# Optimization experiments

Hardware: AMD Instinct MI355X
Metric: run time of the kernel (lower is better)

The kernel has to match this reference:

```python
import jax, jax.numpy as jnp
import numpy as np

B, S, D, H = 2, 2048, 1024, 16
HD = D // H
NEG = -10000.0


def setup_inputs() -> dict:
    key = jax.random.key(0)
    ks = jax.random.split(key, 9)
    # xavier-uniform-like scale for square d_model x d_model weights
    lim = float(np.sqrt(6.0 / (D + D)))
    mk_w = lambda k: jax.random.uniform(k, (D, D), jnp.float32, -lim, lim)
    return {
        "q": jax.random.normal(ks[0], (B, S, D), jnp.float32),
        "k": jax.random.normal(ks[1], (B, S, D), jnp.float32),
        "v": jax.random.normal(ks[2], (B, S, D), jnp.float32),
        "attn_mask": jax.random.randint(ks[3], (B, S), 0, 2, jnp.int32),
        "Wq": mk_w(ks[4]),
        "Wk": mk_w(ks[5]),
        "Wv": mk_w(ks[6]),
        "Wo": mk_w(ks[7]),
        "mask_future": 1,
    }


def reference(q, k, v, attn_mask, Wq, Wk, Wv, Wo, mask_future):
    # nn.Linear(bias=False): y = x @ W.T
    def split_heads(x, W):
        return (x @ W.T).reshape(B, S, H, HD).transpose(0, 2, 1, 3)  # [B,H,S,HD]

    qh = split_heads(q, Wq)
    kh = split_heads(k, Wk)
    vh = split_heads(v, Wv)

    scale = 1.0 / np.sqrt(HD)
    scores = jnp.einsum("bhld,bhsd->bhls", qh, kh) * scale  # [B,H,L,S]

    if mask_future:  # static python flag
        rows = jnp.arange(S)[:, None]
        cols = jnp.arange(S)[None, :]
        causal_bias = jnp.where(cols > rows, jnp.float32(NEG), jnp.float32(0.0))
        scores = scores + causal_bias

    # masked_fill(attn_mask == 0, -10000): sets score exactly to NEG (after bias add)
    pad = attn_mask[:, None, None, :]  # [B,1,1,S]
    scores = jnp.where(pad == 0, jnp.float32(NEG), scores)

    probs = jax.nn.softmax(scores, axis=-1)
    ctx = jnp.einsum("bhls,bhsd->bhld", probs, vh)  # [B,H,L,HD]
    ctx = ctx.transpose(0, 2, 1, 3).reshape(B, S, D)
    return ctx @ Wo.T
```

## Files before the change

kernel.cpp:

```cpp
#include <hip/hip_runtime.h>
#include <hip/hip_bf16.h>

typedef __attribute__((ext_vector_type(8))) short bf16x8;
typedef __attribute__((ext_vector_type(4))) short bf16x4;
typedef __attribute__((ext_vector_type(4))) float f32x4;

#define B_ 2
#define S_ 2048
#define D_ 1024
#define H_ 16
#define HD_ 64
#define M_ 4096
#define NEGV (-10000.0f)

#define NQ_ 4194304
#define NW_ 1048576

#if __has_builtin(__builtin_amdgcn_mfma_f32_16x16x16bf16_1k)
#define HAVE_MFMA16 1
#else
#define HAVE_MFMA16 0
#endif

static __device__ __forceinline__ unsigned short f2bf(float x) {
  __hip_bfloat16 h = __float2bfloat16(x);
  return *reinterpret_cast<unsigned short*>(&h);
}

static __device__ __forceinline__ float bf2f(unsigned short u) {
  unsigned int x = ((unsigned int)u) << 16;
  return __uint_as_float(x);
}

static __device__ __forceinline__ bf16x8 cvt8(const float* p) {
  float4 a = *reinterpret_cast<const float4*>(p);
  float4 b = *reinterpret_cast<const float4*>(p + 4);
  bf16x8 r;
  r[0] = (short)f2bf(a.x); r[1] = (short)f2bf(a.y);
  r[2] = (short)f2bf(a.z); r[3] = (short)f2bf(a.w);
  r[4] = (short)f2bf(b.x); r[5] = (short)f2bf(b.y);
  r[6] = (short)f2bf(b.z); r[7] = (short)f2bf(b.w);
  return r;
}

static __device__ __forceinline__ void gl_lds16(const unsigned short* g, unsigned short* l) {
#if __has_builtin(__builtin_amdgcn_global_load_lds)
  __builtin_amdgcn_global_load_lds(
      (const __attribute__((address_space(1))) unsigned int*)g,
      (__attribute__((address_space(3))) unsigned int*)l, 16, 0, 0);
#else
  *reinterpret_cast<bf16x8*>(l) = *reinterpret_cast<const bf16x8*>(g);
#endif
}


__global__ __launch_bounds__(256) void cvt_all(const float* __restrict__ q,
                                               const float* __restrict__ k,
                                               const float* __restrict__ v,
                                               const float* __restrict__ wq,
                                               const float* __restrict__ wk,
                                               const float* __restrict__ wv,
                                               const float* __restrict__ wo,
                                               unsigned short* __restrict__ dst) {
  for (size_t c = (size_t)blockIdx.x * 256 + threadIdx.x; c < 2097152; c += (size_t)2048 * 256) {
    const size_t e = c * 8;
    const float* s;
    if (e < (size_t)NQ_)            s = q  + e;
    else if (e < (size_t)2 * NQ_)   s = k  + (e - (size_t)NQ_);
    else if (e < (size_t)3 * NQ_)   s = v  + (e - (size_t)2 * NQ_);
    else if (e < (size_t)3 * NQ_ + NW_)     s = wq + (e - (size_t)3 * NQ_);
    else if (e < (size_t)3 * NQ_ + 2 * NW_) s = wk + (e - (size_t)3 * NQ_ - NW_);
    else if (e < (size_t)3 * NQ_ + 3 * NW_) s = wv + (e - (size_t)3 * NQ_ - 2 * NW_);
    else                                    s = wo + (e - (size_t)3 * NQ_ - 3 * NW_);
    *reinterpret_cast<bf16x8*>(dst + e) = cvt8(s);
  }
}

template<bool HSPLIT>
static __device__ __forceinline__ void core_fast(const unsigned short* A,
                                                 const unsigned short* Bw,
                                                 unsigned short* Asm, unsigned short* Bsm,
                                                 int m0, int n0, f32x4 (*acc)[4]) {
  const int tid = threadIdx.x, lane = tid & 63, wid = tid >> 6;
  const int wm = wid >> 1, wn = wid & 1;
  const int l15 = lane & 15, l4 = lane >> 4;

  for (int k0 = 0; k0 < 1024; k0 += 64) {
    __syncthreads();
#pragma unroll
    for (int i = 0; i < 4; ++i) {
      const int idx = tid + 256 * i;
      const int row = idx >> 3;
      const int ce = ((idx & 7) * 8) ^ ((row & 7) << 3);
      const unsigned short* ga;
      if constexpr (HSPLIT) {
        const int m = m0 + row, kk = k0 + ce;
        const int bb = m >> 11, s = m & 2047;
        ga = A + (((size_t)(bb * H_ + (kk >> 6)) * S_ + s) * HD_ + (kk & 63));
      } else {
        ga = A + (size_t)(m0 + row) * 1024 + k0 + ce;
      }
      gl_lds16(ga, Asm + (size_t)idx * 8);
      gl_lds16(Bw + (size_t)(n0 + row) * 1024 + k0 + ce, Bsm + (size_t)idx * 8);
    }
    __syncthreads();
#pragma unroll
    for (int kk = 0; kk < 2; ++kk) {
      bf16x8 af[4], bfr[4];
#pragma unroll
      for (int f = 0; f < 4; ++f) {
        const int ra = wm * 64 + f * 16 + l15;
        const int ca = (kk * 32 + l4 * 8) ^ ((ra & 7) << 3);
        af[f] = *reinterpret_cast<const bf16x8*>(&Asm[ra * 64 + ca]);
        const int rb = wn * 64 + f * 16 + l15;
        const int cb = (kk * 32 + l4 * 8) ^ ((rb & 7) << 3);
        bfr[f] = *reinterpret_cast<const bf16x8*>(&Bsm[rb * 64 + cb]);
      }
#pragma unroll
      for (int fm = 0; fm < 4; ++fm)
#pragma unroll
        for (int fn = 0; fn < 4; ++fn)
          acc[fm][fn] = __builtin_amdgcn_mfma_f32_16x16x32_bf16(af[fm], bfr[fn], acc[fm][fn], 0, 0, 0);
    }
  }
}

__global__ __launch_bounds__(256) void gemm_qkv_fast(const unsigned short* __restrict__ qbf,
                                                     const unsigned short* __restrict__ kbf,
                                                     const unsigned short* __restrict__ vbf,
                                                     const unsigned short* __restrict__ wbf,
                                                     unsigned short* __restrict__ Qh,
                                                     unsigned short* __restrict__ Kh,
                                                     unsigned short* __restrict__ Vt) {
  __shared__ unsigned short Asm[128 * 64];
  __shared__ unsigned short Bsm[128 * 64];
  const int z = blockIdx.z;
  const unsigned short* A  = (z == 0) ? qbf : (z == 1) ? kbf : vbf;
  const unsigned short* Bw = wbf + (size_t)z * NW_;
  const int m0 = blockIdx.y * 128, n0 = blockIdx.x * 128;
  const int lane = threadIdx.x & 63, wid = threadIdx.x >> 6;
  const int wm = wid >> 1, wn = wid & 1;
  const int l15 = lane & 15, l4 = lane >> 4;
  f32x4 acc[4][4] = {};
  core_fast<false>(A, Bw, Asm, Bsm, m0, n0, acc);

#pragma unroll
  for (int fm = 0; fm < 4; ++fm) {
#pragma unroll
    for (int fn = 0; fn < 4; ++fn) {
      const int mg0 = m0 + wm * 64 + fm * 16 + l4 * 4;
      const int ng  = n0 + wn * 64 + fn * 16 + l15;
      const int bidx = mg0 >> 11, s = mg0 & 2047;
      const int h = ng >> 6, d = ng & 63;
      if (z < 2) {
        unsigned short* C = (z == 0) ? Qh : Kh;
#pragma unroll
        for (int r = 0; r < 4; ++r)
          C[((size_t)((bidx * H_ + h) * S_ + s + r)) * HD_ + d] = f2bf(acc[fm][fn][r]);
      } else {
        ushort4 pk;
        pk.x = f2bf(acc[fm][fn][0]); pk.y = f2bf(acc[fm][fn][1]);
        pk.z = f2bf(acc[fm][fn][2]); pk.w = f2bf(acc[fm][fn][3]);
        *reinterpret_cast<ushort4*>(&Vt[((size_t)((bidx * H_ + h) * HD_ + d)) * S_ + s]) = pk;
      }
    }
  }
}

__global__ __launch_bounds__(256) void gemm_o_fast(const unsigned short* __restrict__ ctx,
                                                   const unsigned short* __restrict__ wobf,
                                                   float* __restrict__ Cout) {
  __shared__ unsigned short Asm[128 * 64];
  __shared__ unsigned short Bsm[128 * 64];
  const int m0 = blockIdx.y * 128, n0 = blockIdx.x * 128;
  const int lane = threadIdx.x & 63, wid = threadIdx.x >> 6;
  const int wm = wid >> 1, wn = wid & 1;
  const int l15 = lane & 15, l4 = lane >> 4;
  f32x4 acc[4][4] = {};
  core_fast<true>(ctx, wobf, Asm, Bsm, m0, n0, acc);

#pragma unroll
  for (int fm = 0; fm < 4; ++fm)
#pragma unroll
    for (int fn = 0; fn < 4; ++fn) {
      const int mg0 = m0 + wm * 64 + fm * 16 + l4 * 4;
      const int ng  = n0 + wn * 64 + fn * 16 + l15;
#pragma unroll
      for (int r = 0; r < 4; ++r)
        Cout[(size_t)(mg0 + r) * 1024 + ng] = acc[fm][fn][r];
    }
}

__global__ __launch_bounds__(128) void attn_split(const unsigned short* __restrict__ Qh,
                                                  const unsigned short* __restrict__ Kh,
                                                  const unsigned short* __restrict__ Vt,
                                                  const int* __restrict__ attn_mask,
                                                  const int* __restrict__ mask_future,
                                                  float* __restrict__ Pml,
                                                  unsigned short* __restrict__ Po) {
  constexpr int KVB = 64;
  __shared__ unsigned short Ksm[64 * 64];
  __shared__ unsigned short Vsm[64 * 64];
  __shared__ int s_any;
  const int bx = (int)blockIdx.x;
  int qt, part, bh;
  if (bx < 512)       { part = 0; qt = 16 + (bx >> 5); bh = bx & 31; }
  else if (bx < 544)  { part = 0; qt = 15;             bh = bx & 31; }
  else if (bx < 576)  { part = 1; qt = 31;             bh = bx & 31; }
  else if (bx < 1536) { const int j = bx - 576, g = j >> 6, n = 15 - g, r = j & 63;
                        if (r < 32) { part = 0; qt = n - 1;  bh = r; }
                        else        { part = 1; qt = n + 15; bh = r - 32; } }
  else                { const int j = bx - 1536; part = 1; qt = j >> 5; bh = j & 31; }

  const int q0 = qt * 64;
  const int tid = threadIdx.x, lane = tid & 63, wid = tid >> 6;
  const int l15 = lane & 15, l4 = lane >> 4;
  const int b = bh >> 4;
  const bool causal = (mask_future[0] != 0);
  const int* mrow = attn_mask + b * S_;

  if (tid == 0) s_any = 0;
  __syncthreads();
  for (int i = tid; i <= q0; i += 128)
    if (mrow[i]) s_any = 1;
  __syncthreads();
  const int kb_end_full = (causal && s_any) ? (q0 + 64) : S_;
  const int kb_lo = part ? 1024 : 0;
  const int kb_hi = part ? kb_end_full : (kb_end_full < 1024 ? kb_end_full : 1024);

  const unsigned short* Qb = Qh + (size_t)bh * S_ * HD_;
  const unsigned short* Kb = Kh + (size_t)bh * S_ * HD_;
  const unsigned short* Vb = Vt + (size_t)bh * HD_ * S_;

  float m_run[2] = {-1e30f, -1e30f}, l_run[2] = {0.f, 0.f};
  f32x4 o[2][4] = {};

  if (kb_lo < kb_hi) {
    int qrow[2];
    bf16x8 qf0[2], qf1[2];
#pragma unroll
    for (int f = 0; f < 2; ++f) {
      qrow[f] = q0 + wid * 32 + f * 16 + l15;
      qf0[f] = *reinterpret_cast<const bf16x8*>(&Qb[(size_t)qrow[f] * HD_ + l4 * 8]);
      qf1[f] = *reinterpret_cast<const bf16x8*>(&Qb[(size_t)qrow[f] * HD_ + 32 + l4 * 8]);
    }

    bf16x8 kreg[4], vreg[4];
#pragma unroll
    for (int j = 0; j < 4; ++j) {
      const int idx = tid + 128 * j;
      const int row = idx >> 3;
      const int ce = ((idx & 7) * 8) ^ ((row & 7) << 3);
      kreg[j] = *reinterpret_cast<const bf16x8*>(&Kb[(size_t)(kb_lo + row) * HD_ + ce]);
      vreg[j] = *reinterpret_cast<const bf16x8*>(&Vb[(size_t)row * S_ + kb_lo + ce]);
    }

    for (int kb = kb_lo; kb < kb_hi; kb += KVB) {
      __syncthreads();
#pragma unroll
      for (int j = 0; j < 4; ++j) {
        const int idx = tid + 128 * j;
        *reinterpret_cast<bf16x8*>(&Ksm[idx * 8]) = kreg[j];
        *reinterpret_cast<bf16x8*>(&Vsm[idx * 8]) = vreg[j];
      }
      __syncthreads();

      if (kb + KVB < kb_hi) {
        const int kn = kb + KVB;
#pragma unroll
        for (int j = 0; j < 4; ++j) {
          const int idx = tid + 128 * j;
          const int row = idx >> 3;
          const int ce = ((idx & 7) * 8) ^ ((row & 7) << 3);
          kreg[j] = *reinterpret_cast<const bf16x8*>(&Kb[(size_t)(kn + row) * HD_ + ce]);
          vreg[j] = *reinterpret_cast<const bf16x8*>(&Vb[(size_t)row * S_ + kn + ce]);
        }
      }

      int4 mk4[4];
#pragma unroll
      for (int nf = 0; nf < 4; ++nf)
        mk4[nf] = *reinterpret_cast<const int4*>(&mrow[kb + nf * 16 + l4 * 4]);

#pragma unroll
      for (int f = 0; f < 2; ++f) {
        f32x4 sc[4];
#pragma unroll
        for (int nf = 0; nf < 4; ++nf) {
          const int ra = nf * 16 + l15, sw = (ra & 7) << 3;
          bf16x8 kf0 = *reinterpret_cast<const bf16x8*>(&Ksm[ra * 64 + ((l4 * 8) ^ sw)]);
          bf16x8 kf1 = *reinterpret_cast<const bf16x8*>(&Ksm[ra * 64 + ((32 + l4 * 8) ^ sw)]);
          f32x4 z = {};
          z = __builtin_amdgcn_mfma_f32_16x16x32_bf16(kf0, qf0[f], z, 0, 0, 0);
          z = __builtin_amdgcn_mfma_f32_16x16x32_bf16(kf1, qf1[f], z, 0, 0, 0);
          sc[nf] = z;
        }

        float p[4][4];
        float mx = -1e30f;
#pragma unroll
        for (int nf = 0; nf < 4; ++nf) {
          const int kbase = kb + nf * 16 + l4 * 4;
#pragma unroll
          for (int r = 0; r < 4; ++r) {
            float vv = sc[nf][r] * 0.125f;
            if (causal && (kbase + r) > qrow[f]) vv += NEGV;
            const int mkr = (r == 0) ? mk4[nf].x : (r == 1) ? mk4[nf].y : (r == 2) ? mk4[nf].z : mk4[nf].w;
            if (mkr == 0) vv = NEGV;
            p[nf][r] = vv;
            mx = fmaxf(mx, vv);
          }
        }
        mx = fmaxf(mx, __shfl_xor(mx, 16));
        mx = fmaxf(mx, __shfl_xor(mx, 32));
        const float m_new = fmaxf(m_run[f], mx);
        const float scale = __expf(m_run[f] - m_new);
        float s_loc = 0.f;
#pragma unroll
        for (int nf = 0; nf < 4; ++nf)
#pragma unroll
          for (int r = 0; r < 4; ++r) {
            float e = __expf(p[nf][r] - m_new);
            p[nf][r] = e;
            s_loc += e;
          }
        s_loc += __shfl_xor(s_loc, 16);
        s_loc += __shfl_xor(s_loc, 32);
        l_run[f] = l_run[f] * scale + s_loc;
        m_run[f] = m_new;

        float sq[4];
#pragma unroll
        for (int r = 0; r < 4; ++r) sq[r] = __shfl(scale, l4 * 4 + r);
#pragma unroll
        for (int nf2 = 0; nf2 < 4; ++nf2)
#pragma unroll
          for (int r = 0; r < 4; ++r) o[f][nf2][r] *= sq[r];

        bf16x4 pk[4];
#pragma unroll
        for (int nf = 0; nf < 4; ++nf) {
          bf16x4 t;
          t[0] = (short)f2bf(p[nf][0]); t[1] = (short)f2bf(p[nf][1]);
          t[2] = (short)f2bf(p[nf][2]); t[3] = (short)f2bf(p[nf][3]);
          pk[nf] = t;
        }
#pragma unroll
        for (int nf2 = 0; nf2 < 4; ++nf2) {
          const int rv = nf2 * 16 + l15, swv = (rv & 7) << 3;
#pragma unroll
          for (int nf = 0; nf < 4; ++nf) {
            bf16x4 vf = *reinterpret_cast<const bf16x4*>(&Vsm[rv * 64 + ((nf * 16 + l4 * 4) ^ swv)]);
            o[f][nf2] = __builtin_amdgcn_mfma_f32_16x16x16bf16_1k(pk[nf], vf, o[f][nf2], 0, 0, 0);
          }
        }
      }
    }
  }

#pragma unroll
  for (int f = 0; f < 2; ++f) {
    const int row0 = q0 + wid * 32 + f * 16;
    if (l4 == 0) {
      float* pml = &Pml[(((size_t)bh * S_ + row0 + l15) * 2 + part) * 2];
      pml[0] = m_run[f];
      pml[1] = l_run[f];
    }
#pragma unroll
    for (int nf2 = 0; nf2 < 4; ++nf2)
#pragma unroll
      for (int r = 0; r < 4; ++r) {
        const int row = row0 + l4 * 4 + r;
        Po[(((size_t)bh * S_ + row) * 2 + part) * 64 + nf2 * 16 + l15] = f2bf(o[f][nf2][r]);
      }
  }
}

__global__ __launch_bounds__(256) void attn_combine(const float* __restrict__ Pml,
                                                    const unsigned short* __restrict__ Po,
                                                    unsigned short* __restrict__ ctx) {
  const int t = (int)blockIdx.x * 256 + (int)threadIdx.x;
  const int d = t & 63;
  const size_t rb = (size_t)(t >> 6);
  const float mA = Pml[(rb * 2 + 0) * 2], lA = Pml[(rb * 2 + 0) * 2 + 1];
  const float mB = Pml[(rb * 2 + 1) * 2], lB = Pml[(rb * 2 + 1) * 2 + 1];
  const float ms = fmaxf(mA, mB);
  const float wA = __expf(mA - ms), wB = __expf(mB - ms);
  const float L = lA * wA + lB * wB;
  const float oA = bf2f(Po[(rb * 2 + 0) * 64 + d]);
  const float oB = bf2f(Po[(rb * 2 + 1) * 64 + d]);
  ctx[rb * 64 + d] = f2bf((oA * wA + oB * wB) / L);
}


template<bool AF32, bool BF32, bool HSPLIT>
static __device__ __forceinline__ void gemm_core(const void* Av, const void* Bv,
                                                 unsigned short* Asm, unsigned short* Bsm,
                                                 int m0, int n0, f32x4 (*acc)[4]) {
  constexpr int BK = 64, LDT = 72;
  constexpr int K = 1024;
  const int tid = threadIdx.x;
  const int lane = tid & 63, wid = tid >> 6;
  const int wm = wid >> 1, wn = wid & 1;
  const int l15 = lane & 15, l4 = lane >> 4;

  for (int k0 = 0; k0 < K; k0 += BK) {
    __syncthreads();
#pragma unroll
    for (int i = 0; i < 4; ++i) {
      int idx = tid + 256 * i;
      int row = idx >> 3, k8 = (idx & 7) * 8;
      bf16x8 va, vb;
      if constexpr (AF32) {
        va = cvt8((const float*)Av + (size_t)(m0 + row) * K + k0 + k8);
      } else if constexpr (HSPLIT) {
        const int m = m0 + row, kk = k0 + k8;
        const int bb = m >> 11, s = m & 2047;
        va = *reinterpret_cast<const bf16x8*>(
            (const unsigned short*)Av +
            (((size_t)(bb * H_ + (kk >> 6)) * S_ + s) * HD_ + (kk & 63)));
      } else {
        va = *reinterpret_cast<const bf16x8*>((const unsigned short*)Av + (size_t)(m0 + row) * K + k0 + k8);
      }
      if constexpr (BF32) {
        vb = cvt8((const float*)Bv + (size_t)(n0 + row) * K + k0 + k8);
      } else {
        vb = *reinterpret_cast<const bf16x8*>((const unsigned short*)Bv + (size_t)(n0 + row) * K + k0 + k8);
      }
      *reinterpret_cast<bf16x8*>(&Asm[row * LDT + k8]) = va;
      *reinterpret_cast<bf16x8*>(&Bsm[row * LDT + k8]) = vb;
    }
    __syncthreads();
#pragma unroll
    for (int kk = 0; kk < 2; ++kk) {
      bf16x8 af[4], bfr[4];
#pragma unroll
      for (int f = 0; f < 4; ++f) {
        af[f]  = *reinterpret_cast<const bf16x8*>(&Asm[(wm * 64 + f * 16 + l15) * LDT + kk * 32 + l4 * 8]);
        bfr[f] = *reinterpret_cast<const bf16x8*>(&Bsm[(wn * 64 + f * 16 + l15) * LDT + kk * 32 + l4 * 8]);
      }
#pragma unroll
      for (int fm = 0; fm < 4; ++fm)
#pragma unroll
        for (int fn = 0; fn < 4; ++fn)
          acc[fm][fn] = __builtin_amdgcn_mfma_f32_16x16x32_bf16(af[fm], bfr[fn], acc[fm][fn], 0, 0, 0);
    }
  }
}

__global__ __launch_bounds__(256) void gemm_qkv3(const float* __restrict__ q,
                                                 const float* __restrict__ k,
                                                 const float* __restrict__ v,
                                                 const float* __restrict__ Wq,
                                                 const float* __restrict__ Wk,
                                                 const float* __restrict__ Wv,
                                                 unsigned short* __restrict__ Qh,
                                                 unsigned short* __restrict__ Kh,
                                                 unsigned short* __restrict__ Vt) {
  constexpr int LDT = 72;
  __shared__ unsigned short Asm[128 * LDT];
  __shared__ unsigned short Bsm[128 * LDT];
  const int z = blockIdx.z;
  const float* A  = (z == 0) ? q  : (z == 1) ? k  : v;
  const float* Bw = (z == 0) ? Wq : (z == 1) ? Wk : Wv;
  const int m0 = blockIdx.y * 128, n0 = blockIdx.x * 128;
  const int lane = threadIdx.x & 63, wid = threadIdx.x >> 6;
  const int wm = wid >> 1, wn = wid & 1;
  const int l15 = lane & 15, l4 = lane >> 4;
  f32x4 acc[4][4] = {};
  gemm_core<true, true, false>(A, Bw, Asm, Bsm, m0, n0, acc);

#pragma unroll
  for (int fm = 0; fm < 4; ++fm) {
#pragma unroll
    for (int fn = 0; fn < 4; ++fn) {
      const int mg0 = m0 + wm * 64 + fm * 16 + l4 * 4;
      const int ng  = n0 + wn * 64 + fn * 16 + l15;
      const int bidx = mg0 >> 11, s = mg0 & 2047;
      const int h = ng >> 6, d = ng & 63;
      if (z < 2) {
        unsigned short* C = (z == 0) ? Qh : Kh;
#pragma unroll
        for (int r = 0; r < 4; ++r)
          C[((size_t)((bidx * H_ + h) * S_ + s + r)) * HD_ + d] = f2bf(acc[fm][fn][r]);
      } else {
        ushort4 pk;
        pk.x = f2bf(acc[fm][fn][0]); pk.y = f2bf(acc[fm][fn][1]);
        pk.z = f2bf(acc[fm][fn][2]); pk.w = f2bf(acc[fm][fn][3]);
        *reinterpret_cast<ushort4*>(&Vt[((size_t)((bidx * H_ + h) * HD_ + d)) * S_ + s]) = pk;
      }
    }
  }
}

__global__ __launch_bounds__(256) void gemm_oproj(const void* __restrict__ Av,
                                                  const void* __restrict__ Bv,
                                                  float* __restrict__ Cout) {
  constexpr int LDT = 72;
  __shared__ unsigned short Asm[128 * LDT];
  __shared__ unsigned short Bsm[128 * LDT];
  const int m0 = blockIdx.y * 128, n0 = blockIdx.x * 128;
  const int lane = threadIdx.x & 63, wid = threadIdx.x >> 6;
  const int wm = wid >> 1, wn = wid & 1;
  const int l15 = lane & 15, l4 = lane >> 4;
  f32x4 acc[4][4] = {};
  gemm_core<false, true, true>(Av, Bv, Asm, Bsm, m0, n0, acc);

#pragma unroll
  for (int fm = 0; fm < 4; ++fm)
#pragma unroll
    for (int fn = 0; fn < 4; ++fn) {
      const int mg0 = m0 + wm * 64 + fm * 16 + l4 * 4;
      const int ng  = n0 + wn * 64 + fn * 16 + l15;
#pragma unroll
      for (int r = 0; r < 4; ++r)
        Cout[(size_t)(mg0 + r) * 1024 + ng] = acc[fm][fn][r];
    }
}

__global__ __launch_bounds__(128) void attn_fwd(const unsigned short* Qh,
                                                const unsigned short* __restrict__ Kh,
                                                const unsigned short* __restrict__ Vt,
                                                const int* __restrict__ attn_mask,
                                                const int* __restrict__ mask_future,
                                                unsigned short* ctx) {
  constexpr int KVB = 64;
  __shared__ unsigned short Ksm[64 * 64];
  __shared__ unsigned short Vsm[64 * 64];
  __shared__ int s_any;
  const int tid = threadIdx.x, lane = tid & 63, wid = tid >> 6;
  const int l15 = lane & 15, l4 = lane >> 4;
  const int bh = blockIdx.y, b = bh >> 4;
  const int q0 = (int)((blockIdx.x + 9 * blockIdx.y) & 31) * 64;
  const bool causal = (mask_future[0] != 0);
  const int* mrow = attn_mask + b * S_;

  if (tid == 0) s_any = 0;
  __syncthreads();
  for (int i = tid; i <= q0; i += 128)
    if (mrow[i]) s_any = 1;
  __syncthreads();
  const int kb_end = (causal && s_any) ? (q0 + 64) : S_;

  const unsigned short* Qb = Qh + (size_t)bh * S_ * HD_;
  const unsigned short* Kb = Kh + (size_t)bh * S_ * HD_;
  const unsigned short* Vb = Vt + (size_t)bh * HD_ * S_;

  int qrow[2];
  bf16x8 qf0[2], qf1[2];
#pragma unroll
  for (int f = 0; f < 2; ++f) {
    qrow[f] = q0 + wid * 32 + f * 16 + l15;
    qf0[f] = *reinterpret_cast<const bf16x8*>(&Qb[(size_t)qrow[f] * HD_ + l4 * 8]);
    qf1[f] = *reinterpret_cast<const bf16x8*>(&Qb[(size_t)qrow[f] * HD_ + 32 + l4 * 8]);
  }

  float m_run[2] = {-1e30f, -1e30f}, l_run[2] = {0.f, 0.f};
  f32x4 o[2][4] = {};

  bf16x8 kreg[4], vreg[4];
#pragma unroll
  for (int j = 0; j < 4; ++j) {
    const int idx = tid + 128 * j;
    const int row = idx >> 3;
    const int ce = ((idx & 7) * 8) ^ ((row & 7) << 3);
    kreg[j] = *reinterpret_cast<const bf16x8*>(&Kb[(size_t)row * HD_ + ce]);
    vreg[j] = *reinterpret_cast<const bf16x8*>(&Vb[(size_t)row * S_ + ce]);
  }

  for (int kb = 0; kb < kb_end; kb += KVB) {
    __syncthreads();
#pragma unroll
    for (int j = 0; j < 4; ++j) {
      const int idx = tid + 128 * j;
      *reinterpret_cast<bf16x8*>(&Ksm[idx * 8]) = kreg[j];
      *reinterpret_cast<bf16x8*>(&Vsm[idx * 8]) = vreg[j];
    }
    __syncthreads();

    if (kb + KVB < kb_end) {
      const int kn = kb + KVB;
#pragma unroll
      for (int j = 0; j < 4; ++j) {
        const int idx = tid + 128 * j;
        const int row = idx >> 3;
        const int ce = ((idx & 7) * 8) ^ ((row & 7) << 3);
        kreg[j] = *reinterpret_cast<const bf16x8*>(&Kb[(size_t)(kn + row) * HD_ + ce]);
        vreg[j] = *reinterpret_cast<const bf16x8*>(&Vb[(size_t)row * S_ + kn + ce]);
      }
    }

    int4 mk4[4];
#pragma unroll
    for (int nf = 0; nf < 4; ++nf)
      mk4[nf] = *reinterpret_cast<const int4*>(&mrow[kb + nf * 16 + l4 * 4]);

#pragma unroll
    for (int f = 0; f < 2; ++f) {
      f32x4 sc[4];
#pragma unroll
      for (int nf = 0; nf < 4; ++nf) {
        const int ra = nf * 16 + l15, sw = (ra & 7) << 3;
        bf16x8 kf0 = *reinterpret_cast<const bf16x8*>(&Ksm[ra * 64 + ((l4 * 8) ^ sw)]);
        bf16x8 kf1 = *reinterpret_cast<const bf16x8*>(&Ksm[ra * 64 + ((32 + l4 * 8) ^ sw)]);
        f32x4 z = {};
        z = __builtin_amdgcn_mfma_f32_16x16x32_bf16(kf0, qf0[f], z, 0, 0, 0);
        z = __builtin_amdgcn_mfma_f32_16x16x32_bf16(kf1, qf1[f], z, 0, 0, 0);
        sc[nf] = z;
      }

      float p[4][4];
      float mx = -1e30f;
#pragma unroll
      for (int nf = 0; nf < 4; ++nf) {
        const int kbase = kb + nf * 16 + l4 * 4;
#pragma unroll
        for (int r = 0; r < 4; ++r) {
          float vv = sc[nf][r] * 0.125f;
          if (causal && (kbase + r) > qrow[f]) vv += NEGV;
          const int mkr = (r == 0) ? mk4[nf].x : (r == 1) ? mk4[nf].y : (r == 2) ? mk4[nf].z : mk4[nf].w;
          if (mkr == 0) vv = NEGV;
          p[nf][r] = vv;
          mx = fmaxf(mx, vv);
        }
      }
      mx = fmaxf(mx, __shfl_xor(mx, 16));
      mx = fmaxf(mx, __shfl_xor(mx, 32));
      const float m_new = fmaxf(m_run[f], mx);
      const float scale = __expf(m_run[f] - m_new);
      float s_loc = 0.f;
#pragma unroll
      for (int nf = 0; nf < 4; ++nf)
#pragma unroll
        for (int r = 0; r < 4; ++r) {
          float e = __expf(p[nf][r] - m_new);
          p[nf][r] = e;
          s_loc += e;
        }
      s_loc += __shfl_xor(s_loc, 16);
      s_loc += __shfl_xor(s_loc, 32);
      l_run[f] = l_run[f] * scale + s_loc;
      m_run[f] = m_new;

      float sq[4];
#pragma unroll
      for (int r = 0; r < 4; ++r) sq[r] = __shfl(scale, l4 * 4 + r);
#pragma unroll
      for (int nf2 = 0; nf2 < 4; ++nf2)
#pragma unroll
        for (int r = 0; r < 4; ++r) o[f][nf2][r] *= sq[r];

      bf16x4 pk[4];
#pragma unroll
      for (int nf = 0; nf < 4; ++nf) {
        bf16x4 t;
        t[0] = (short)f2bf(p[nf][0]); t[1] = (short)f2bf(p[nf][1]);
        t[2] = (short)f2bf(p[nf][2]); t[3] = (short)f2bf(p[nf][3]);
        pk[nf] = t;
      }
#pragma unroll
      for (int nf2 = 0; nf2 < 4; ++nf2) {
        const int rv = nf2 * 16 + l15, swv = (rv & 7) << 3;
#pragma unroll
        for (int nf = 0; nf < 4; ++nf) {
          bf16x4 vf = *reinterpret_cast<const bf16x4*>(&Vsm[rv * 64 + ((nf * 16 + l4 * 4) ^ swv)]);
          o[f][nf2] = __builtin_amdgcn_mfma_f32_16x16x16bf16_1k(pk[nf], vf, o[f][nf2], 0, 0, 0);
        }
      }
    }
  }

#pragma unroll
  for (int f = 0; f < 2; ++f) {
    const float linv = 1.f / l_run[f];
    float lq[4];
#pragma unroll
    for (int r = 0; r < 4; ++r) lq[r] = __shfl(linv, l4 * 4 + r);
#pragma unroll
    for (int nf2 = 0; nf2 < 4; ++nf2)
#pragma unroll
      for (int r = 0; r < 4; ++r) {
        const int rowg = q0 + wid * 32 + f * 16 + l4 * 4 + r;
        ctx[((size_t)bh * S_ + rowg) * HD_ + nf2 * 16 + l15] = f2bf(o[f][nf2][r] * lq[r]);
      }
  }
}

extern "C" void kernel_launch(void* const* d_in, const int* in_sizes, int n_in,
                              void* d_out, int out_size, void* d_ws, size_t ws_size,
                              hipStream_t stream) {
  const float* q = (const float*)d_in[0];
  const float* k = (const float*)d_in[1];
  const float* v = (const float*)d_in[2];
  const int* attn_mask = (const int*)d_in[3];
  const float* Wq = (const float*)d_in[4];
  const float* Wk = (const float*)d_in[5];
  const float* Wv = (const float*)d_in[6];
  const float* Wo = (const float*)d_in[7];
  const int* mask_future = (const int*)d_in[8];

  unsigned short* ws = (unsigned short*)d_ws;
  unsigned short* Vt = (unsigned short*)d_out;
  float* out = (float*)d_out;
  (void)in_sizes; (void)n_in; (void)out_size;

  const size_t CVT_ELEMS = (size_t)3 * NQ_ + 4 * NW_;
  const size_t NEED = (CVT_ELEMS + 2 * (size_t)NQ_) * 2;

  if (ws_size >= NEED) {
    unsigned short* cvt = ws;
    unsigned short* qbf = cvt;
    unsigned short* kbf = cvt + (size_t)NQ_;
    unsigned short* vbf = cvt + (size_t)2 * NQ_;
    unsigned short* wbf = cvt + (size_t)3 * NQ_;
    unsigned short* Qh  = cvt + CVT_ELEMS;
    unsigned short* Kh  = Qh + (size_t)NQ_;
    float* Pml = (float*)d_ws;
    unsigned short* Po = (unsigned short*)((char*)d_ws + (1 << 20));

    cvt_all<<<2048, 256, 0, stream>>>(q, k, v, Wq, Wk, Wv, Wo, cvt);
    gemm_qkv_fast<<<dim3(8, 32, 3), 256, 0, stream>>>(qbf, kbf, vbf, wbf, Qh, Kh, Vt);
    attn_split<<<2048, 128, 0, stream>>>(Qh, Kh, Vt, attn_mask, mask_future, Pml, Po);
    attn_combine<<<16384, 256, 0, stream>>>(Pml, Po, Qh);
    gemm_o_fast<<<dim3(8, 32), 256, 0, stream>>>(Qh, wbf + (size_t)3 * NW_, out);
  } else {
    unsigned short* Qh = ws;
    unsigned short* Kh = ws + (size_t)NQ_;
    gemm_qkv3<<<dim3(8, 32, 3), 256, 0, stream>>>(q, k, v, Wq, Wk, Wv, Qh, Kh, Vt);
    attn_fwd<<<dim3(32, 32), 128, 0, stream>>>(Qh, Kh, Vt, attn_mask, mask_future, Qh);
    gemm_oproj<<<dim3(8, 32), 256, 0, stream>>>(Qh, Wo, out);
  }
}
```

Measured before the change: 175.8 us.

## Use atomic work queue and three-way KV split in attention

The attention kernel now pulls jobs from a global atomic counter instead of mapping a fixed job to each block. A separate tiny kernel zeroes the counter before launch. The KV range is split into three 768-key chunks rather than two halves, and jobs are ordered longest-first to balance the causal workload across CUs. The combine kernel merges three partial softmax states instead of two, and the partial buffers are relocated into the dead bf16 input region. The cost is more partial-result traffic, atomic contention and an extra launch.

```diff
diff --git a/kernel.cpp b/kernel.cpp
--- a/kernel.cpp
+++ b/kernel.cpp
@@ -15,12 +15,7 @@
 
 #define NQ_ 4194304
 #define NW_ 1048576
-
-#if __has_builtin(__builtin_amdgcn_mfma_f32_16x16x16bf16_1k)
-#define HAVE_MFMA16 1
-#else
-#define HAVE_MFMA16 0
-#endif
+#define NJOBS 3072
 
 static __device__ __forceinline__ unsigned short f2bf(float x) {
   __hip_bfloat16 h = __float2bfloat16(x);
@@ -191,188 +186,200 @@
     }
 }
 
+__global__ void zero_ctr(unsigned int* c) { *c = 0; }
+
 __global__ __launch_bounds__(128) void attn_split(const unsigned short* __restrict__ Qh,
                                                   const unsigned short* __restrict__ Kh,
                                                   const unsigned short* __restrict__ Vt,
                                                   const int* __restrict__ attn_mask,
                                                   const int* __restrict__ mask_future,
                                                   float* __restrict__ Pml,
-                                                  unsigned short* __restrict__ Po) {
+                                                  unsigned short* __restrict__ Po,
+                                                  unsigned int* __restrict__ ctr) {
   constexpr int KVB = 64;
   __shared__ unsigned short Ksm[64 * 64];
   __shared__ unsigned short Vsm[64 * 64];
-  __shared__ int s_any;
-  const int bx = (int)blockIdx.x;
-  int qt, part, bh;
-  if (bx < 512)       { part = 0; qt = 16 + (bx >> 5); bh = bx & 31; }
-  else if (bx < 544)  { part = 0; qt = 15;             bh = bx & 31; }
-  else if (bx < 576)  { part = 1; qt = 31;             bh = bx & 31; }
-  else if (bx < 1536) { const int j = bx - 576, g = j >> 6, n = 15 - g, r = j & 63;
-                        if (r < 32) { part = 0; qt = n - 1;  bh = r; }
-                        else        { part = 1; qt = n + 15; bh = r - 32; } }
-  else                { const int j = bx - 1536; part = 1; qt = j >> 5; bh = j & 31; }
-
-  const int q0 = qt * 64;
+  __shared__ int s_job, s_any;
   const int tid = threadIdx.x, lane = tid & 63, wid = tid >> 6;
   const int l15 = lane & 15, l4 = lane >> 4;
-  const int b = bh >> 4;
   const bool causal = (mask_future[0] != 0);
-  const int* mrow = attn_mask + b * S_;
-
-  if (tid == 0) s_any = 0;
-  __syncthreads();
-  for (int i = tid; i <= q0; i += 128)
-    if (mrow[i]) s_any = 1;
-  __syncthreads();
-  const int kb_end_full = (causal && s_any) ? (q0 + 64) : S_;
-  const int kb_lo = part ? 1024 : 0;
-  const int kb_hi = part ? kb_end_full : (kb_end_full < 1024 ? kb_end_full : 1024);
-
-  const unsigned short* Qb = Qh + (size_t)bh * S_ * HD_;
-  const unsigned short* Kb = Kh + (size_t)bh * S_ * HD_;
-  const unsigned short* Vb = Vt + (size_t)bh * HD_ * S_;
-
-  float m_run[2] = {-1e30f, -1e30f}, l_run[2] = {0.f, 0.f};
-  f32x4 o[2][4] = {};
-
-  if (kb_lo < kb_hi) {
-    int qrow[2];
-    bf16x8 qf0[2], qf1[2];
-#pragma unroll
-    for (int f = 0; f < 2; ++f) {
-      qrow[f] = q0 + wid * 32 + f * 16 + l15;
-      qf0[f] = *reinterpret_cast<const bf16x8*>(&Qb[(size_t)qrow[f] * HD_ + l4 * 8]);
-      qf1[f] = *reinterpret_cast<const bf16x8*>(&Qb[(size_t)qrow[f] * HD_ + 32 + l4 * 8]);
-    }
-
-    bf16x8 kreg[4], vreg[4];
-#pragma unroll
-    for (int j = 0; j < 4; ++j) {
-      const int idx = tid + 128 * j;
-      const int row = idx >> 3;
-      const int ce = ((idx & 7) * 8) ^ ((row & 7) << 3);
-      kreg[j] = *reinterpret_cast<const bf16x8*>(&Kb[(size_t)(kb_lo + row) * HD_ + ce]);
-      vreg[j] = *reinterpret_cast<const bf16x8*>(&Vb[(size_t)row * S_ + kb_lo + ce]);
-    }
-
-    for (int kb = kb_lo; kb < kb_hi; kb += KVB) {
-      __syncthreads();
-#pragma unroll
-      for (int j = 0; j < 4; ++j) {
-        const int idx = tid + 128 * j;
-        *reinterpret_cast<bf16x8*>(&Ksm[idx * 8]) = kreg[j];
-        *reinterpret_cast<bf16x8*>(&Vsm[idx * 8]) = vreg[j];
-      }
-      __syncthreads();
-
-      if (kb + KVB < kb_hi) {
-        const int kn = kb + KVB;
-#pragma unroll
-        for (int j = 0; j < 4; ++j) {
-          const int idx = tid + 128 * j;
-          const int row = idx >> 3;
-          const int ce = ((idx & 7) * 8) ^ ((row & 7) << 3);
-          kreg[j] = *reinterpret_cast<const bf16x8*>(&Kb[(size_t)(kn + row) * HD_ + ce]);
-          vreg[j] = *reinterpret_cast<const bf16x8*>(&Vb[(size_t)row * S_ + kn + ce]);
+
+  for (;;) {
+    __syncthreads();
+    if (tid == 0) s_job = (int)atomicAdd(ctr, 1u);
+    __syncthreads();
+    const int g = s_job;
+    if (g >= NJOBS) break;
+    const int bh = g & 31, j = g >> 5, b = bh >> 4;
+
+    int qt, p;
+    if (j < 21)      { p = 0; qt = 11 + j; }
+    else if (j < 30) { p = 1; qt = 2 + j; }
+    else if (j < 36) { const int L = 11 - ((j - 30) >> 1); p = (j - 30) & 1;
+                       qt = p ? 11 + L : L - 1; }
+    else if (j < 60) { const int jj = j - 36, L = 8 - jj / 3, pp = jj % 3;
+                       p = pp; qt = (pp == 0) ? L - 1 : (pp == 1) ? 11 + L : 23 + L; }
+    else if (j < 72) { p = 1; qt = j - 60; }
+    else             { p = 2; qt = j - 72; }
+
+    const int q0 = qt * 64;
+    const int* mrow = attn_mask + b * S_;
+
+    if (tid == 0) s_any = 0;
+    __syncthreads();
+    for (int i = tid; i <= q0; i += 128)
+      if (mrow[i]) s_any = 1;
+    __syncthreads();
+    const int kb_end_full = (causal && s_any) ? (q0 + 64) : S_;
+    const int kb_lo = p * 768;
+    const int kb_hi = (kb_lo + 768 < kb_end_full) ? (kb_lo + 768) : kb_end_full;
+
+    const unsigned short* Qb = Qh + (size_t)bh * S_ * HD_;
+    const unsigned short* Kb = Kh + (size_t)bh * S_ * HD_;
+    const unsigned short* Vb = Vt + (size_t)bh * HD_ * S_;
+
+    float m_run[2] = {-1e30f, -1e30f}, l_run[2] = {0.f, 0.f};
+    f32x4 o[2][4] = {};
+
+    if (kb_lo < kb_hi) {
+      int qrow[2];
+      bf16x8 qf0[2], qf1[2];
+#pragma unroll
+      for (int f = 0; f < 2; ++f) {
+        qrow[f] = q0 + wid * 32 + f * 16 + l15;
+        qf0[f] = *reinterpret_cast<const bf16x8*>(&Qb[(size_t)qrow[f] * HD_ + l4 * 8]);
+        qf1[f] = *reinterpret_cast<const bf16x8*>(&Qb[(size_t)qrow[f] * HD_ + 32 + l4 * 8]);
+      }
+
+      bf16x8 kreg[4], vreg[4];
+#pragma unroll
+      for (int jj = 0; jj < 4; ++jj) {
+        const int idx = tid + 128 * jj;
+        const int row = idx >> 3;
+        const int ce = ((idx & 7) * 8) ^ ((row & 7) << 3);
+        kreg[jj] = *reinterpret_cast<const bf16x8*>(&Kb[(size_t)(kb_lo + row) * HD_ + ce]);
+        vreg[jj] = *reinterpret_cast<const bf16x8*>(&Vb[(size_t)row * S_ + kb_lo + ce]);
+      }
+
+      for (int kb = kb_lo; kb < kb_hi; kb += KVB) {
+        __syncthreads();
+#pragma unroll
+        for (int jj = 0; jj < 4; ++jj) {
+          const int idx = tid + 128 * jj;
+          *reinterpret_cast<bf16x8*>(&Ksm[idx * 8]) = kreg[jj];
+          *reinterpret_cast<bf16x8*>(&Vsm[idx * 8]) = vreg[jj];
         }
-      }
-
-      int4 mk4[4];
-#pragma unroll
-      for (int nf = 0; nf < 4; ++nf)
-        mk4[nf] = *reinterpret_cast<const int4*>(&mrow[kb + nf * 16 + l4 * 4]);
-
-#pragma unroll
-      for (int f = 0; f < 2; ++f) {
-        f32x4 sc[4];
-#pragma unroll
-        for (int nf = 0; nf < 4; ++nf) {
-          const int ra = nf * 16 + l15, sw = (ra & 7) << 3;
-          bf16x8 kf0 = *reinterpret_cast<const bf16x8*>(&Ksm[ra * 64 + ((l4 * 8) ^ sw)]);
-          bf16x8 kf1 = *reinterpret_cast<const bf16x8*>(&Ksm[ra * 64 + ((32 + l4 * 8) ^ sw)]);
-          f32x4 z = {};
-          z = __builtin_amdgcn_mfma_f32_16x16x32_bf16(kf0, qf0[f], z, 0, 0, 0);
-          z = __builtin_amdgcn_mfma_f32_16x16x32_bf16(kf1, qf1[f], z, 0, 0, 0);
-          sc[nf] = z;
-        }
-
-        float p[4][4];
-        float mx = -1e30f;
-#pragma unroll
-        for (int nf = 0; nf < 4; ++nf) {
-          const int kbase = kb + nf * 16 + l4 * 4;
-#pragma unroll
-          for (int r = 0; r < 4; ++r) {
-            float vv = sc[nf][r] * 0.125f;
-            if (causal && (kbase + r) > qrow[f]) vv += NEGV;
-            const int mkr = (r == 0) ? mk4[nf].x : (r == 1) ? mk4[nf].y : (r == 2) ? mk4[nf].z : mk4[nf].w;
-            if (mkr == 0) vv = NEGV;
-            p[nf][r] = vv;
-            mx = fmaxf(mx, vv);
+        __syncthreads();
+
+        if (kb + KVB < kb_hi) {
+          const int kn = kb + KVB;
+#pragma unroll
+          for (int jj = 0; jj < 4; ++jj) {
+            const int idx = tid + 128 * jj;
+            const int row = idx >> 3;
+            const int ce = ((idx & 7) * 8) ^ ((row & 7) << 3);
+            kreg[jj] = *reinterpret_cast<const bf16x8*>(&Kb[(size_t)(kn + row) * HD_ + ce]);
+            vreg[jj] = *reinterpret_cast<const bf16x8*>(&Vb[(size_t)row * S_ + kn + ce]);
           }
         }
-        mx = fmaxf(mx, __shfl_xor(mx, 16));
-        mx = fmaxf(mx, __shfl_xor(mx, 32));
-        const float m_new = fmaxf(m_run[f], mx);
-        const float scale = __expf(m_run[f] - m_new);
-        float s_loc = 0.f;
+
+        int4 mk4[4];
 #pragma unroll
         for (int nf = 0; nf < 4; ++nf)
-#pragma unroll
-          for (int r = 0; r < 4; ++r) {
-            float e = __expf(p[nf][r] - m_new);
-            p[nf][r] = e;
-            s_loc += e;
+          mk4[nf] = *reinterpret_cast<const int4*>(&mrow[kb + nf * 16 + l4 * 4]);
+
+#pragma unroll
+        for (int f = 0; f < 2; ++f) {
+          f32x4 sc[4];
+#pragma unroll
+          for (int nf = 0; nf < 4; ++nf) {
+            const int ra = nf * 16 + l15, sw = (ra & 7) << 3;
+            bf16x8 kf0 = *reinterpret_cast<const bf16x8*>(&Ksm[ra * 64 + ((l4 * 8) ^ sw)]);
+            bf16x8 kf1 = *reinterpret_cast<const bf16x8*>(&Ksm[ra * 64 + ((32 + l4 * 8) ^ sw)]);
+            f32x4 z = {};
+            z = __builtin_amdgcn_mfma_f32_16x16x32_bf16(kf0, qf0[f], z, 0, 0, 0);
+            z = __builtin_amdgcn_mfma_f32_16x16x32_bf16(kf1, qf1[f], z, 0, 0, 0);
+            sc[nf] = z;
           }
-        s_loc += __shfl_xor(s_loc, 16);
-        s_loc += __shfl_xor(s_loc, 32);
-        l_run[f] = l_run[f] * scale + s_loc;
-        m_run[f] = m_new;
-
-        float sq[4];
-#pragma unroll
-        for (int r = 0; r < 4; ++r) sq[r] = __shfl(scale, l4 * 4 + r);
-#pragma unroll
-        for (int nf2 = 0; nf2 < 4; ++nf2)
-#pragma unroll
-          for (int r = 0; r < 4; ++r) o[f][nf2][r] *= sq[r];
-
-        bf16x4 pk[4];
-#pragma unroll
-        for (int nf = 0; nf < 4; ++nf) {
-          bf16x4 t;
-          t[0] = (short)f2bf(p[nf][0]); t[1] = (short)f2bf(p[nf][1]);
-          t[2] = (short)f2bf(p[nf][2]); t[3] = (short)f2bf(p[nf][3]);
-          pk[nf] = t;
-        }
-#pragma unroll
-        for (int nf2 = 0; nf2 < 4; ++nf2) {
-          const int rv = nf2 * 16 + l15, swv = (rv & 7) << 3;
+
+          float pp_[4][4];
+          float mx = -1e30f;
 #pragma unroll
           for (int nf = 0; nf < 4; ++nf) {
-            bf16x4 vf = *reinterpret_cast<const bf16x4*>(&Vsm[rv * 64 + ((nf * 16 + l4 * 4) ^ swv)]);
-            o[f][nf2] = __builtin_amdgcn_mfma_f32_16x16x16bf16_1k(pk[nf], vf, o[f][nf2], 0, 0, 0);
+            const int kbase = kb + nf * 16 + l4 * 4;
+#pragma unroll
+            for (int r = 0; r < 4; ++r) {
+              float vv = sc[nf][r] * 0.125f;
+              if (causal && (kbase + r) > qrow[f]) vv += NEGV;
+              const int mkr = (r == 0) ? mk4[nf].x : (r == 1) ? mk4[nf].y : (r == 2) ? mk4[nf].z : mk4[nf].w;
+              if (mkr == 0) vv = NEGV;
+              pp_[nf][r] = vv;
+              mx = fmaxf(mx, vv);
+            }
+          }
+          mx = fmaxf(mx, __shfl_xor(mx, 16));
+          mx = fmaxf(mx, __shfl_xor(mx, 32));
+          const float m_new = fmaxf(m_run[f], mx);
+          const float scale = __expf(m_run[f] - m_new);
+          float s_loc = 0.f;
+#pragma unroll
+          for (int nf = 0; nf < 4; ++nf)
+#pragma unroll
+            for (int r = 0; r < 4; ++r) {
+              float e = __expf(pp_[nf][r] - m_new);
+              pp_[nf][r] = e;
+              s_loc += e;
+            }
+          s_loc += __shfl_xor(s_loc, 16);
+          s_loc += __shfl_xor(s_loc, 32);
+          l_run[f] = l_run[f] * scale + s_loc;
+          m_run[f] = m_new;
+
+          float sq[4];
+#pragma unroll
+          for (int r = 0; r < 4; ++r) sq[r] = __shfl(scale, l4 * 4 + r);
+#pragma unroll
+          for (int nf2 = 0; nf2 < 4; ++nf2)
+#pragma unroll
+            for (int r = 0; r < 4; ++r) o[f][nf2][r] *= sq[r];
+
+          bf16x4 pk[4];
+#pragma unroll
+          for (int nf = 0; nf < 4; ++nf) {
+            bf16x4 t;
+            t[0] = (short)f2bf(pp_[nf][0]); t[1] = (short)f2bf(pp_[nf][1]);
+            t[2] = (short)f2bf(pp_[nf][2]); t[3] = (short)f2bf(pp_[nf][3]);
+            pk[nf] = t;
+          }
+#pragma unroll
+          for (int nf2 = 0; nf2 < 4; ++nf2) {
+            const int rv = nf2 * 16 + l15, swv = (rv & 7) << 3;
+#pragma unroll
+            for (int nf = 0; nf < 4; ++nf) {
+              bf16x4 vf = *reinterpret_cast<const bf16x4*>(&Vsm[rv * 64 + ((nf * 16 + l4 * 4) ^ swv)]);
+              o[f][nf2] = __builtin_amdgcn_mfma_f32_16x16x16bf16_1k(pk[nf], vf, o[f][nf2], 0, 0, 0);
+            }
           }
         }
       }
     }
-  }
-
-#pragma unroll
-  for (int f = 0; f < 2; ++f) {
-    const int row0 = q0 + wid * 32 + f * 16;
-    if (l4 == 0) {
-      float* pml = &Pml[(((size_t)bh * S_ + row0 + l15) * 2 + part) * 2];
-      pml[0] = m_run[f];
-      pml[1] = l_run[f];
-    }
-#pragma unroll
-    for (int nf2 = 0; nf2 < 4; ++nf2)
-#pragma unroll
-      for (int r = 0; r < 4; ++r) {
-        const int row = row0 + l4 * 4 + r;
-        Po[(((size_t)bh * S_ + row) * 2 + part) * 64 + nf2 * 16 + l15] = f2bf(o[f][nf2][r]);
-      }
+
+#pragma unroll
+    for (int f = 0; f < 2; ++f) {
+      const int row0 = q0 + wid * 32 + f * 16;
+      if (l4 == 0) {
+        float* pml = &Pml[(((size_t)bh * S_ + row0 + l15) * 3 + p) * 2];
+        pml[0] = m_run[f];
+        pml[1] = l_run[f];
+      }
+#pragma unroll
+      for (int nf2 = 0; nf2 < 4; ++nf2)
+#pragma unroll
+        for (int r = 0; r < 4; ++r) {
+          const int row = row0 + l4 * 4 + r;
+          Po[(((size_t)bh * S_ + row) * 3 + p) * 64 + nf2 * 16 + l15] = f2bf(o[f][nf2][r]);
+        }
+    }
   }
 }
 
@@ -382,14 +389,16 @@
   const int t = (int)blockIdx.x * 256 + (int)threadIdx.x;
   const int d = t & 63;
   const size_t rb = (size_t)(t >> 6);
-  const float mA = Pml[(rb * 2 + 0) * 2], lA = Pml[(rb * 2 + 0) * 2 + 1];
-  const float mB = Pml[(rb * 2 + 1) * 2], lB = Pml[(rb * 2 + 1) * 2 + 1];
-  const float ms = fmaxf(mA, mB);
-  const float wA = __expf(mA - ms), wB = __expf(mB - ms);
-  const float L = lA * wA + lB * wB;
-  const float oA = bf2f(Po[(rb * 2 + 0) * 64 + d]);
-  const float oB = bf2f(Po[(rb * 2 + 1) * 64 + d]);
-  ctx[rb * 64 + d] = f2bf((oA * wA + oB * wB) / L);
+  const float m0v = Pml[(rb * 3 + 0) * 2], l0 = Pml[(rb * 3 + 0) * 2 + 1];
+  const float m1v = Pml[(rb * 3 + 1) * 2], l1 = Pml[(rb * 3 + 1) * 2 + 1];
+  const float m2v = Pml[(rb * 3 + 2) * 2], l2 = Pml[(rb * 3 + 2) * 2 + 1];
+  const float ms = fmaxf(fmaxf(m0v, m1v), m2v);
+  const float w0 = __expf(m0v - ms), w1 = __expf(m1v - ms), w2 = __expf(m2v - ms);
+  const float L = l0 * w0 + l1 * w1 + l2 * w2;
+  const float o0 = bf2f(Po[(rb * 3 + 0) * 64 + d]);
+  const float o1 = bf2f(Po[(rb * 3 + 1) * 64 + d]);
+  const float o2 = bf2f(Po[(rb * 3 + 2) * 64 + d]);
+  ctx[rb * 64 + d] = f2bf((o0 * w0 + o1 * w1 + o2 * w2) / L);
 }
 
 
@@ -715,12 +724,14 @@
     unsigned short* wbf = cvt + (size_t)3 * NQ_;
     unsigned short* Qh  = cvt + CVT_ELEMS;
     unsigned short* Kh  = Qh + (size_t)NQ_;
-    float* Pml = (float*)d_ws;
-    unsigned short* Po = (unsigned short*)((char*)d_ws + (1 << 20));
+    unsigned short* Po = cvt;
+    float* Pml = (float*)(cvt + (size_t)3 * NQ_);
+    unsigned int* ctr = (unsigned int*)(Pml + (size_t)32 * 2048 * 3 * 2);
 
     cvt_all<<<2048, 256, 0, stream>>>(q, k, v, Wq, Wk, Wv, Wo, cvt);
     gemm_qkv_fast<<<dim3(8, 32, 3), 256, 0, stream>>>(qbf, kbf, vbf, wbf, Qh, Kh, Vt);
-    attn_split<<<2048, 128, 0, stream>>>(Qh, Kh, Vt, attn_mask, mask_future, Pml, Po);
+    zero_ctr<<<1, 1, 0, stream>>>(ctr);
+    attn_split<<<2048, 128, 0, stream>>>(Qh, Kh, Vt, attn_mask, mask_future, Pml, Po, ctr);
     attn_combine<<<16384, 256, 0, stream>>>(Pml, Po, Qh);
     gemm_o_fast<<<dim3(8, 32), 256, 0, stream>>>(Qh, wbf + (size_t)3 * NW_, out);
   } else {
```

New measurement: 222.7 us. 26.7% more time.
